# Kernel tuning notes

Measured on AMD Instinct MI355X. Metric: run time of the kernel, lower is better.

The kernel has to match this reference:

```python
import jax, jax.numpy as jnp
import numpy as np

EMBD_DIM = 1024
HEAD_SIZE = 64


def setup_inputs() -> dict:
    key = jax.random.key(0)
    kx, kq, kk, kv = jax.random.split(key, 4)
    x = jax.random.normal(kx, (4, 4096, EMBD_DIM), dtype=jnp.float32)
    # nn.Linear(embd_dim, head_size, bias=False) weights, stored as [C, H] so x @ W
    s = 1.0 / np.sqrt(EMBD_DIM)
    Wq = jax.random.uniform(kq, (EMBD_DIM, HEAD_SIZE), jnp.float32, -s, s)
    Wk = jax.random.uniform(kk, (EMBD_DIM, HEAD_SIZE), jnp.float32, -s, s)
    Wv = jax.random.uniform(kv, (EMBD_DIM, HEAD_SIZE), jnp.float32, -s, s)
    return {"x": x, "Wq": Wq, "Wk": Wk, "Wv": Wv}


def reference(x, Wq, Wk, Wv):
    # q,k,v: [B, T, H]
    q = jnp.einsum("btc,ch->bth", x, Wq)
    k = jnp.einsum("btc,ch->bth", x, Wk)
    v = jnp.einsum("btc,ch->bth", x, Wv)
    scale = k.shape[-1] ** -0.5
    # full [B, T, T] score matrix, as in the original naive implementation
    scores = jnp.einsum("bth,bsh->bts", q, k) * scale
    attn = jax.nn.softmax(scores, axis=-1)
    # dropout p=0.0 -> identity
    out = jnp.einsum("bts,bsh->bth", attn, v)  # [B, T, H]
    return out
```

## Files before the change

kernel.cpp:

```cpp
#include <hip/hip_runtime.h>
#include <hip/hip_bf16.h>

#define B_ 4
#define T_ 4096
#define C_ 1024
#define H_ 64

typedef float  f32x4  __attribute__((ext_vector_type(4)));
typedef short  bf16x8 __attribute__((ext_vector_type(8)));
typedef uint   u32x4  __attribute__((ext_vector_type(4)));

static __device__ __forceinline__ ushort f2bf(float f) {
  union { float f; uint u; } v; v.f = f;
  uint u = v.u;
  u += 0x7FFFu + ((u >> 16) & 1u);
  return (ushort)(u >> 16);
}

static __device__ __forceinline__ uint cvtpk(float s0, float s1) {
  uint r;
  asm("v_cvt_pk_bf16_f32 %0, %1, %2" : "=v"(r) : "v"(s0), "v"(s1));
  return r;
}

static __device__ __forceinline__ void gload_lds16(const void* g, void* l) {
  __builtin_amdgcn_global_load_lds(
      (const __attribute__((address_space(1))) unsigned int*)g,
      (__attribute__((address_space(3))) unsigned int*)l, 16, 0, 0);
}

#define MFMA(a, b, c) __builtin_amdgcn_mfma_f32_16x16x32_bf16(a, b, c, 0, 0, 0)

__global__ __launch_bounds__(256) void wt_prep(const float* __restrict__ Wq,
                                               const float* __restrict__ Wk,
                                               const float* __restrict__ Wv,
                                               ushort* __restrict__ WtF) {
  int idx = blockIdx.x * 256 + threadIdx.x;
  int j = idx & 7, lane = (idx >> 3) & 63, nt = (idx >> 9) & 3;
  int kc = (idx >> 11) & 1, c64 = (idx >> 12) & 15, w = idx >> 16;
  int l15 = lane & 15, g = lane >> 4;
  int c = c64 * 64 + kc * 32 + g * 8 + j;
  int n = nt * 16 + l15;
  const float* W = (w == 0) ? Wq : (w == 1) ? Wk : Wv;
  WtF[idx] = f2bf(W[c * 64 + n]);
}

__global__ __launch_bounds__(256) void qkv_proj(const float* __restrict__ x,
                                                const ushort* __restrict__ WtF,
                                                ushort* __restrict__ Qg,
                                                char* __restrict__ KaF,
                                                char* __restrict__ VaF) {
  __shared__ __align__(16) ushort wl[2][12288];
  const int tid = threadIdx.x;
  const int lane = tid & 63, wid = tid >> 6;
  const int l15 = lane & 15, g = lane >> 4;
  const int b = blockIdx.x >> 6, rt = blockIdx.x & 63;
  const int wrow = rt * 64 + wid * 16;

  f32x4 acc[3][4];
  #pragma unroll
  for (int w = 0; w < 3; w++)
    #pragma unroll
    for (int nt = 0; nt < 4; nt++) acc[w][nt] = (f32x4)0.0f;

  const float* xr = x + ((size_t)b * T_ + wrow + l15) * C_ + g * 8;

  auto stagew = [&](int buf, int c64) {
    char* dst = (char*)wl[buf] + tid * 16;
    const char* src = (const char*)WtF + (size_t)c64 * 8192 + tid * 16;
    #pragma unroll
    for (int p = 0; p < 6; p++)
      gload_lds16(src + (p >> 1) * 131072 + (p & 1) * 4096, dst + p * 4096);
  };

  f32x4 xp[3][4];
  auto xload = [&](int slot, int t) {
    const float* src = xr + t * 64;
    xp[slot][0] = *(const f32x4*)src;
    xp[slot][1] = *(const f32x4*)(src + 4);
    xp[slot][2] = *(const f32x4*)(src + 32);
    xp[slot][3] = *(const f32x4*)(src + 36);
  };

  stagew(0, 0);
  xload(0, 0);
  xload(1, 1);
  asm volatile("s_waitcnt vmcnt(8)" ::: "memory");
  __builtin_amdgcn_s_barrier();
  __builtin_amdgcn_sched_barrier(0);

  #pragma unroll
  for (int t = 0; t < 16; t++) {
    const int cur = t & 1;
    if (t < 15) stagew(cur ^ 1, t + 1);
    if (t < 14) xload((t + 2) % 3, t + 2);

    const int slot = t % 3;
    bf16x8 xa[2];
    #pragma unroll
    for (int kc = 0; kc < 2; kc++) {
      union { uint u[4]; bf16x8 v; } h;
      f32x4 c0 = xp[slot][2 * kc], c1 = xp[slot][2 * kc + 1];
      h.u[0] = cvtpk(c0[0], c0[1]); h.u[1] = cvtpk(c0[2], c0[3]);
      h.u[2] = cvtpk(c1[0], c1[1]); h.u[3] = cvtpk(c1[2], c1[3]);
      xa[kc] = h.v;
    }
    const char* wb = (const char*)wl[cur] + lane * 16;
    __builtin_amdgcn_s_setprio(1);
    #pragma unroll
    for (int w = 0; w < 3; w++)
      #pragma unroll
      for (int kc = 0; kc < 2; kc++)
        #pragma unroll
        for (int nt = 0; nt < 4; nt++) {
          bf16x8 wf = *(const bf16x8*)(wb + w * 8192 + kc * 4096 + nt * 1024);
          acc[w][nt] = MFMA(xa[kc], wf, acc[w][nt]);
        }
    __builtin_amdgcn_s_setprio(0);

    if (t < 15) {
      if (t < 14) asm volatile("s_waitcnt vmcnt(4)" ::: "memory");
      else        asm volatile("s_waitcnt vmcnt(0)" ::: "memory");
      __builtin_amdgcn_s_barrier();
      __builtin_amdgcn_sched_barrier(0);
    }
  }

  char* kdst = KaF + ((size_t)b * 64 + rt) * 8192;
  char* vdst = VaF + ((size_t)b * 128 + (wrow >> 5)) * 4096;
  #pragma unroll
  for (int nt = 0; nt < 4; nt++) {
    int n = nt * 16 + l15;
    int kc = n >> 5, gp2 = (n >> 3) & 3, j2 = n & 7;
    #pragma unroll
    for (int r = 0; r < 4; r++) {
      int tt = wrow + g * 4 + r;
      Qg[((size_t)b * T_ + tt) * H_ + n] = f2bf(acc[0][nt][r]);
      int key = tt & 63;
      *(ushort*)(kdst + kc * 4096 + (key >> 4) * 1024 +
                 (gp2 * 16 + (key & 15)) * 16 + j2 * 2) = f2bf(acc[1][nt][r]);
      int k5 = tt & 31;
      int gp = ((k5 >> 4) << 1) | ((k5 >> 2) & 1);
      int js = ((k5 >> 3) & 1) * 4 + (k5 & 3);
      *(ushort*)(vdst + nt * 1024 + (gp * 16 + l15) * 16 + js * 2) = f2bf(acc[2][nt][r]);
    }
  }
}

__global__ __launch_bounds__(256, 2) void attn(const ushort* __restrict__ Qg,
                                               const char* __restrict__ KaF,
                                               const char* __restrict__ VaF,
                                               float* __restrict__ Op,
                                               float* __restrict__ Ds,
                                               float* __restrict__ out,
                                               int KT) {
  const int tid = threadIdx.x;
  const int lane = tid & 63, wid = tid >> 6;
  const int bid = blockIdx.x;
  const int b = bid & 3;
  const int r2 = bid >> 2;
  const int qt = r2 & 31, s = r2 >> 5;
  const int l15 = lane & 15, g = lane >> 4;

  bf16x8 qa[2][2];
  #pragma unroll
  for (int qs = 0; qs < 2; qs++) {
    const ushort* qp = Qg + ((size_t)b * T_ + qt * 128 + wid * 32 + qs * 16 + l15) * H_ + g * 8;
    qa[qs][0] = *(const bf16x8*)qp;
    qa[qs][1] = *(const bf16x8*)(qp + 32);
  }

  f32x4 oacc[2][4];
  #pragma unroll
  for (int qs = 0; qs < 2; qs++)
    #pragma unroll
    for (int nt = 0; nt < 4; nt++) oacc[qs][nt] = (f32x4)0.0f;
  float dsum[2] = {0.f, 0.f};

  const char* kbase = KaF + (size_t)b * 64 * 8192;
  const char* vbase = VaF + (size_t)b * 128 * 4096;
  const int it0 = s * KT;

  bf16x8 kaA[8], kaB[8];
  {
    const char* kt = kbase + (size_t)it0 * 8192 + lane * 16;
    #pragma unroll
    for (int i = 0; i < 8; i++) kaA[i] = *(const bf16x8*)(kt + i * 1024);
  }

  auto body = [&](int it, bf16x8 (&kaC)[8], bf16x8 (&kaN)[8]) {
    const char* vt = vbase + (size_t)(it0 + it) * 8192 + lane * 16;
    bf16x8 va[8];
    #pragma unroll
    for (int i = 0; i < 8; i++) va[i] = *(const bf16x8*)(vt + i * 1024);

    f32x4 sacc[2][4];
    #pragma unroll
    for (int qs = 0; qs < 2; qs++)
      #pragma unroll
      for (int nt = 0; nt < 4; nt++) sacc[qs][nt] = (f32x4)0.0f;
    __builtin_amdgcn_s_setprio(1);
    #pragma unroll
    for (int nt = 0; nt < 4; nt++)
      #pragma unroll
      for (int qs = 0; qs < 2; qs++) {
        sacc[qs][nt] = MFMA(kaC[nt], qa[qs][0], sacc[qs][nt]);
        sacc[qs][nt] = MFMA(kaC[4 + nt], qa[qs][1], sacc[qs][nt]);
      }
    __builtin_amdgcn_s_setprio(0);

    if (it + 1 < KT) {
      const char* kt = kbase + (size_t)(it0 + it + 1) * 8192 + lane * 16;
      #pragma unroll
      for (int i = 0; i < 8; i++) kaN[i] = *(const bf16x8*)(kt + i * 1024);
    }

    uint t0[2][4], t1[2][4];
    #pragma unroll
    for (int qs = 0; qs < 2; qs++)
      #pragma unroll
      for (int nt = 0; nt < 4; nt++) {
        float p0 = __builtin_amdgcn_exp2f(sacc[qs][nt][0] * 0.18033688011112042f);
        float p1 = __builtin_amdgcn_exp2f(sacc[qs][nt][1] * 0.18033688011112042f);
        float p2 = __builtin_amdgcn_exp2f(sacc[qs][nt][2] * 0.18033688011112042f);
        float p3 = __builtin_amdgcn_exp2f(sacc[qs][nt][3] * 0.18033688011112042f);
        dsum[qs] += (p0 + p1) + (p2 + p3);
        t0[qs][nt] = cvtpk(p0, p1);
        t1[qs][nt] = cvtpk(p2, p3);
      }

    #pragma unroll
    for (int kk = 0; kk < 2; kk++) {
      bf16x8 pf[2];
      #pragma unroll
      for (int qs = 0; qs < 2; qs++) {
        uint x0 = t0[qs][2 * kk], y0 = t0[qs][2 * kk + 1];
        uint x1 = t1[qs][2 * kk], y1 = t1[qs][2 * kk + 1];
        asm volatile("v_permlane32_swap_b32 %0, %1" : "+v"(x0), "+v"(y0));
        asm volatile("v_permlane32_swap_b32 %0, %1" : "+v"(x1), "+v"(y1));
        union { uint u[4]; bf16x8 v; } pfu;
        pfu.u[0] = x0; pfu.u[1] = x1; pfu.u[2] = y0; pfu.u[3] = y1;
        pf[qs] = pfu.v;
      }
      __builtin_amdgcn_s_setprio(1);
      #pragma unroll
      for (int ntd = 0; ntd < 4; ntd++) {
        oacc[0][ntd] = MFMA(va[kk * 4 + ntd], pf[0], oacc[0][ntd]);
        oacc[1][ntd] = MFMA(va[kk * 4 + ntd], pf[1], oacc[1][ntd]);
      }
      __builtin_amdgcn_s_setprio(0);
    }
  };

  for (int it = 0; it < KT; it += 2) {
    body(it, kaA, kaB);
    body(it + 1, kaB, kaA);
  }

  #pragma unroll
  for (int qs = 0; qs < 2; qs++) {
    float d = dsum[qs];
    d += __shfl_xor(d, 16, 64);
    d += __shfl_xor(d, 32, 64);
    const int q = qt * 128 + wid * 32 + qs * 16 + l15;
    if (Op != nullptr) {
      float* ob = Op + ((size_t)(s * 4 + b) * T_ + q) * H_;
      #pragma unroll
      for (int nt = 0; nt < 4; nt++)
        #pragma unroll
        for (int r = 0; r < 4; r++) ob[nt * 16 + g * 4 + r] = oacc[qs][nt][r];
      if (g == 0) Ds[(size_t)(s * 4 + b) * T_ + q] = d;
    } else {
      float inv = 1.0f / d;
      float* ob = out + ((size_t)b * T_ + q) * H_;
      #pragma unroll
      for (int nt = 0; nt < 4; nt++)
        #pragma unroll
        for (int r = 0; r < 4; r++) ob[nt * 16 + g * 4 + r] = oacc[qs][nt][r] * inv;
    }
  }
}

__global__ __launch_bounds__(256) void reduce_seg(const float* __restrict__ Op,
                                                  const float* __restrict__ Ds,
                                                  float* __restrict__ out, int seg) {
  int i = blockIdx.x * 256 + threadIdx.x;
  size_t e = (size_t)i * 4;
  int row = (int)(e >> 6);
  f32x4 o = (f32x4)0.0f;
  float d = 0.0f;
  for (int s = 0; s < seg; s++) {
    o += *(const f32x4*)(Op + (size_t)s * (4u * T_ * H_) + e);
    d += Ds[(size_t)s * (4u * T_) + row];
  }
  *(f32x4*)(out + e) = o * (1.0f / d);
}

extern "C" void kernel_launch(void* const* d_in, const int* in_sizes, int n_in,
                              void* d_out, int out_size, void* d_ws, size_t ws_size,
                              hipStream_t stream) {
  const float* x  = (const float*)d_in[0];
  const float* Wq = (const float*)d_in[1];
  const float* Wk = (const float*)d_in[2];
  const float* Wv = (const float*)d_in[3];
  float* out = (float*)d_out;

  char* ws = (char*)d_ws;
  size_t off = 0;
  auto take = [&](size_t n) -> void* {
    void* p = ws + off;
    off = (off + n + 255) & ~(size_t)255;
    return p;
  };
  ushort* Qg  = (ushort*)take((size_t)B_ * T_ * H_ * 2);
  char*   KaF = (char*)take((size_t)B_ * T_ * H_ * 2);
  char*   VaF = (char*)take((size_t)B_ * T_ * H_ * 2);
  ushort* WtF = (ushort*)take((size_t)3 * H_ * C_ * 2);

  int seg = 1;
  float* Op = nullptr;
  float* Ds = nullptr;
  for (int sg = 4; sg >= 2; sg >>= 1) {
    size_t need = off + (size_t)sg * B_ * T_ * H_ * 4 + 256 + (size_t)sg * B_ * T_ * 4 + 256;
    if (need <= ws_size) {
      seg = sg;
      Op = (float*)take((size_t)sg * B_ * T_ * H_ * 4);
      Ds = (float*)take((size_t)sg * B_ * T_ * 4);
      break;
    }
  }
  int KT = 64 / seg;

  wt_prep<<<768, 256, 0, stream>>>(Wq, Wk, Wv, WtF);
  qkv_proj<<<B_ * 64, 256, 0, stream>>>(x, WtF, Qg, KaF, VaF);
  attn<<<B_ * (T_ / 128) * seg, 256, 0, stream>>>(Qg, KaF, VaF, Op, Ds, out, KT);
  if (Op) reduce_seg<<<(B_ * T_ * H_ / 4 + 255) / 256, 256, 0, stream>>>(Op, Ds, out, seg);
}
```

Baseline: 54.88 us.

## Stage K/V tiles in double-buffered LDS and double per-block query tile

The attention kernel now has each block cover 256 queries, with each wave handling 64, instead of 128. K and V tiles are copied from global memory into a double-buffered LDS area with direct global-to-LDS loads, and waves read their MFMA operands from LDS, so one tile fetch is shared by four waves. The split over key segments rises to 8 when the workspace allows, which keeps the grid large enough. In exchange it adds a barrier and a full vmcnt wait on every iteration, more accumulator registers per wave (which may lower occupancy with launch bounds of 2), and more partial results for the reduction kernel to combine.

```diff
diff --git a/kernel.cpp b/kernel.cpp
--- a/kernel.cpp
+++ b/kernel.cpp
@@ -154,70 +154,74 @@
                                                float* __restrict__ Ds,
                                                float* __restrict__ out,
                                                int KT) {
+  __shared__ __align__(16) char kv[2][16384];
   const int tid = threadIdx.x;
   const int lane = tid & 63, wid = tid >> 6;
   const int bid = blockIdx.x;
   const int b = bid & 3;
-  const int r2 = bid >> 2;
-  const int qt = r2 & 31, s = r2 >> 5;
+  const int qt = (bid >> 2) & 15, s = bid >> 6;
   const int l15 = lane & 15, g = lane >> 4;
 
-  bf16x8 qa[2][2];
-  #pragma unroll
-  for (int qs = 0; qs < 2; qs++) {
-    const ushort* qp = Qg + ((size_t)b * T_ + qt * 128 + wid * 32 + qs * 16 + l15) * H_ + g * 8;
+  bf16x8 qa[4][2];
+  #pragma unroll
+  for (int qs = 0; qs < 4; qs++) {
+    const ushort* qp = Qg + ((size_t)b * T_ + qt * 256 + wid * 64 + qs * 16 + l15) * H_ + g * 8;
     qa[qs][0] = *(const bf16x8*)qp;
     qa[qs][1] = *(const bf16x8*)(qp + 32);
   }
 
-  f32x4 oacc[2][4];
-  #pragma unroll
-  for (int qs = 0; qs < 2; qs++)
+  f32x4 oacc[4][4];
+  #pragma unroll
+  for (int qs = 0; qs < 4; qs++)
     #pragma unroll
     for (int nt = 0; nt < 4; nt++) oacc[qs][nt] = (f32x4)0.0f;
-  float dsum[2] = {0.f, 0.f};
+  float dsum[4] = {0.f, 0.f, 0.f, 0.f};
 
   const char* kbase = KaF + (size_t)b * 64 * 8192;
   const char* vbase = VaF + (size_t)b * 128 * 4096;
   const int it0 = s * KT;
 
-  bf16x8 kaA[8], kaB[8];
-  {
-    const char* kt = kbase + (size_t)it0 * 8192 + lane * 16;
-    #pragma unroll
-    for (int i = 0; i < 8; i++) kaA[i] = *(const bf16x8*)(kt + i * 1024);
-  }
-
-  auto body = [&](int it, bf16x8 (&kaC)[8], bf16x8 (&kaN)[8]) {
-    const char* vt = vbase + (size_t)(it0 + it) * 8192 + lane * 16;
-    bf16x8 va[8];
-    #pragma unroll
-    for (int i = 0; i < 8; i++) va[i] = *(const bf16x8*)(vt + i * 1024);
-
-    f32x4 sacc[2][4];
-    #pragma unroll
-    for (int qs = 0; qs < 2; qs++)
+  auto stage = [&](int buf, int it) {
+    char* dst = kv[buf] + tid * 16;
+    const char* ks = kbase + (size_t)it * 8192 + tid * 16;
+    const char* vs = vbase + (size_t)it * 8192 + tid * 16;
+    gload_lds16(ks, dst);
+    gload_lds16(ks + 4096, dst + 4096);
+    gload_lds16(vs, dst + 8192);
+    gload_lds16(vs + 4096, dst + 12288);
+  };
+
+  stage(0, it0);
+  asm volatile("s_waitcnt vmcnt(0)" ::: "memory");
+  __builtin_amdgcn_s_barrier();
+  __builtin_amdgcn_sched_barrier(0);
+
+  for (int it = 0; it < KT; it++) {
+    const int cur = it & 1;
+    if (it + 1 < KT) stage(cur ^ 1, it0 + it + 1);
+    const char* kl = kv[cur];
+    const char* vl = kv[cur] + 8192;
+
+    f32x4 sacc[4][4];
+    #pragma unroll
+    for (int qs = 0; qs < 4; qs++)
       #pragma unroll
       for (int nt = 0; nt < 4; nt++) sacc[qs][nt] = (f32x4)0.0f;
     __builtin_amdgcn_s_setprio(1);
     #pragma unroll
     for (int nt = 0; nt < 4; nt++)
       #pragma unroll
-      for (int qs = 0; qs < 2; qs++) {
-        sacc[qs][nt] = MFMA(kaC[nt], qa[qs][0], sacc[qs][nt]);
-        sacc[qs][nt] = MFMA(kaC[4 + nt], qa[qs][1], sacc[qs][nt]);
+      for (int kc = 0; kc < 2; kc++) {
+        bf16x8 ka = *(const bf16x8*)(kl + kc * 4096 + nt * 1024 + lane * 16);
+        #pragma unroll
+        for (int qs = 0; qs < 4; qs++)
+          sacc[qs][nt] = MFMA(ka, qa[qs][kc], sacc[qs][nt]);
       }
     __builtin_amdgcn_s_setprio(0);
 
-    if (it + 1 < KT) {
-      const char* kt = kbase + (size_t)(it0 + it + 1) * 8192 + lane * 16;
-      #pragma unroll
-      for (int i = 0; i < 8; i++) kaN[i] = *(const bf16x8*)(kt + i * 1024);
-    }
-
-    uint t0[2][4], t1[2][4];
-    #pragma unroll
-    for (int qs = 0; qs < 2; qs++)
+    uint t0[4][4], t1[4][4];
+    #pragma unroll
+    for (int qs = 0; qs < 4; qs++)
       #pragma unroll
       for (int nt = 0; nt < 4; nt++) {
         float p0 = __builtin_amdgcn_exp2f(sacc[qs][nt][0] * 0.18033688011112042f);
@@ -231,9 +235,9 @@
 
     #pragma unroll
     for (int kk = 0; kk < 2; kk++) {
-      bf16x8 pf[2];
-      #pragma unroll
-      for (int qs = 0; qs < 2; qs++) {
+      bf16x8 pf[4];
+      #pragma unroll
+      for (int qs = 0; qs < 4; qs++) {
         uint x0 = t0[qs][2 * kk], y0 = t0[qs][2 * kk + 1];
         uint x1 = t1[qs][2 * kk], y1 = t1[qs][2 * kk + 1];
         asm volatile("v_permlane32_swap_b32 %0, %1" : "+v"(x0), "+v"(y0));
@@ -245,24 +249,27 @@
       __builtin_amdgcn_s_setprio(1);
       #pragma unroll
       for (int ntd = 0; ntd < 4; ntd++) {
-        oacc[0][ntd] = MFMA(va[kk * 4 + ntd], pf[0], oacc[0][ntd]);
-        oacc[1][ntd] = MFMA(va[kk * 4 + ntd], pf[1], oacc[1][ntd]);
+        bf16x8 va = *(const bf16x8*)(vl + kk * 4096 + ntd * 1024 + lane * 16);
+        #pragma unroll
+        for (int qs = 0; qs < 4; qs++)
+          oacc[qs][ntd] = MFMA(va, pf[qs], oacc[qs][ntd]);
       }
       __builtin_amdgcn_s_setprio(0);
     }
-  };
-
-  for (int it = 0; it < KT; it += 2) {
-    body(it, kaA, kaB);
-    body(it + 1, kaB, kaA);
-  }
-
-  #pragma unroll
-  for (int qs = 0; qs < 2; qs++) {
+
+    if (it + 1 < KT) {
+      asm volatile("s_waitcnt vmcnt(0)" ::: "memory");
+      __builtin_amdgcn_s_barrier();
+      __builtin_amdgcn_sched_barrier(0);
+    }
+  }
+
+  #pragma unroll
+  for (int qs = 0; qs < 4; qs++) {
     float d = dsum[qs];
     d += __shfl_xor(d, 16, 64);
     d += __shfl_xor(d, 32, 64);
-    const int q = qt * 128 + wid * 32 + qs * 16 + l15;
+    const int q = qt * 256 + wid * 64 + qs * 16 + l15;
     if (Op != nullptr) {
       float* ob = Op + ((size_t)(s * 4 + b) * T_ + q) * H_;
       #pragma unroll
@@ -320,7 +327,7 @@
   int seg = 1;
   float* Op = nullptr;
   float* Ds = nullptr;
-  for (int sg = 4; sg >= 2; sg >>= 1) {
+  for (int sg = 8; sg >= 2; sg >>= 1) {
     size_t need = off + (size_t)sg * B_ * T_ * H_ * 4 + 256 + (size_t)sg * B_ * T_ * 4 + 256;
     if (need <= ws_size) {
       seg = sg;
@@ -333,6 +340,6 @@
 
   wt_prep<<<768, 256, 0, stream>>>(Wq, Wk, Wv, WtF);
   qkv_proj<<<B_ * 64, 256, 0, stream>>>(x, WtF, Qg, KaF, VaF);
-  attn<<<B_ * (T_ / 128) * seg, 256, 0, stream>>>(Qg, KaF, VaF, Op, Ds, out, KT);
+  attn<<<B_ * (T_ / 256) * seg, 256, 0, stream>>>(Qg, KaF, VaF, Op, Ds, out, KT);
   if (Op) reduce_seg<<<(B_ * T_ * H_ / 4 + 255) / 256, 256, 0, stream>>>(Op, Ds, out, seg);
 }
```

Result: slower. 60.21 us (+9.7%).

## Stage K/V tiles through LDS with triple-buffered async loads; bf16 partials

Applied to the files above, without the earlier changes.

The attention kernel now copies each K/V tile into a three-slot LDS ring using global_load_lds, staged two iterations ahead, with waitcnt and barriers between iterations. Previously each wave loaded K and V straight into registers. The LDS path shares one tile load across the four waves and cuts VGPR pressure. The split-K partial outputs are now written as bf16 instead of fp32, which halves the traffic to and from reduce_seg but loses some precision. wt_prep is also reorganised so its reads of the weights are coalesced, with the layout transform moved to the write side. The per-iteration barriers add synchronisation cost.

```diff
diff --git a/kernel.cpp b/kernel.cpp
--- a/kernel.cpp
+++ b/kernel.cpp
@@ -36,13 +36,14 @@
                                                const float* __restrict__ Wv,
                                                ushort* __restrict__ WtF) {
   int idx = blockIdx.x * 256 + threadIdx.x;
-  int j = idx & 7, lane = (idx >> 3) & 63, nt = (idx >> 9) & 3;
-  int kc = (idx >> 11) & 1, c64 = (idx >> 12) & 15, w = idx >> 16;
-  int l15 = lane & 15, g = lane >> 4;
-  int c = c64 * 64 + kc * 32 + g * 8 + j;
-  int n = nt * 16 + l15;
+  int w = idx >> 16, idx2 = idx & 65535;
+  int c = idx2 >> 6, n = idx2 & 63;
   const float* W = (w == 0) ? Wq : (w == 1) ? Wk : Wv;
-  WtF[idx] = f2bf(W[c * 64 + n]);
+  float v = W[idx2];
+  int c64 = c >> 6, kc = (c >> 5) & 1, g = (c >> 3) & 3, j = c & 7;
+  int nt = n >> 4, l15 = n & 15;
+  size_t dst = ((size_t)((((w * 16 + c64) * 2 + kc) * 4 + nt) * 64 + g * 16 + l15)) * 8 + j;
+  WtF[dst] = f2bf(v);
 }
 
 __global__ __launch_bounds__(256) void qkv_proj(const float* __restrict__ x,
@@ -150,16 +151,16 @@
 __global__ __launch_bounds__(256, 2) void attn(const ushort* __restrict__ Qg,
                                                const char* __restrict__ KaF,
                                                const char* __restrict__ VaF,
-                                               float* __restrict__ Op,
+                                               ushort* __restrict__ Op,
                                                float* __restrict__ Ds,
                                                float* __restrict__ out,
                                                int KT) {
+  __shared__ __align__(16) char kv[3][16384];
   const int tid = threadIdx.x;
   const int lane = tid & 63, wid = tid >> 6;
   const int bid = blockIdx.x;
   const int b = bid & 3;
-  const int r2 = bid >> 2;
-  const int qt = r2 & 31, s = r2 >> 5;
+  const int qt = (bid >> 2) & 31, s = bid >> 7;
   const int l15 = lane & 15, g = lane >> 4;
 
   bf16x8 qa[2][2];
@@ -181,18 +182,28 @@
   const char* vbase = VaF + (size_t)b * 128 * 4096;
   const int it0 = s * KT;
 
-  bf16x8 kaA[8], kaB[8];
-  {
-    const char* kt = kbase + (size_t)it0 * 8192 + lane * 16;
-    #pragma unroll
-    for (int i = 0; i < 8; i++) kaA[i] = *(const bf16x8*)(kt + i * 1024);
-  }
-
-  auto body = [&](int it, bf16x8 (&kaC)[8], bf16x8 (&kaN)[8]) {
-    const char* vt = vbase + (size_t)(it0 + it) * 8192 + lane * 16;
-    bf16x8 va[8];
-    #pragma unroll
-    for (int i = 0; i < 8; i++) va[i] = *(const bf16x8*)(vt + i * 1024);
+  auto stage = [&](int buf, int it) {
+    char* dst = kv[buf] + tid * 16;
+    const char* ks = kbase + (size_t)it * 8192 + tid * 16;
+    const char* vs = vbase + (size_t)it * 8192 + tid * 16;
+    gload_lds16(ks, dst);
+    gload_lds16(ks + 4096, dst + 4096);
+    gload_lds16(vs, dst + 8192);
+    gload_lds16(vs + 4096, dst + 12288);
+  };
+
+  stage(0, it0);
+  stage(1, it0 + 1);
+  asm volatile("s_waitcnt vmcnt(4)" ::: "memory");
+  __builtin_amdgcn_s_barrier();
+  __builtin_amdgcn_sched_barrier(0);
+
+  int cur = 0;
+  for (int it = 0; it < KT; it++) {
+    int pf = cur + 2; if (pf >= 3) pf -= 3;
+    if (it + 2 < KT) stage(pf, it0 + it + 2);
+    const char* kl = kv[cur];
+    const char* vl = kv[cur] + 8192;
 
     f32x4 sacc[2][4];
     #pragma unroll
@@ -203,17 +214,12 @@
     #pragma unroll
     for (int nt = 0; nt < 4; nt++)
       #pragma unroll
-      for (int qs = 0; qs < 2; qs++) {
-        sacc[qs][nt] = MFMA(kaC[nt], qa[qs][0], sacc[qs][nt]);
-        sacc[qs][nt] = MFMA(kaC[4 + nt], qa[qs][1], sacc[qs][nt]);
+      for (int kc = 0; kc < 2; kc++) {
+        bf16x8 ka = *(const bf16x8*)(kl + kc * 4096 + nt * 1024 + lane * 16);
+        sacc[0][nt] = MFMA(ka, qa[0][kc], sacc[0][nt]);
+        sacc[1][nt] = MFMA(ka, qa[1][kc], sacc[1][nt]);
       }
     __builtin_amdgcn_s_setprio(0);
-
-    if (it + 1 < KT) {
-      const char* kt = kbase + (size_t)(it0 + it + 1) * 8192 + lane * 16;
-      #pragma unroll
-      for (int i = 0; i < 8; i++) kaN[i] = *(const bf16x8*)(kt + i * 1024);
-    }
 
     uint t0[2][4], t1[2][4];
     #pragma unroll
@@ -231,7 +237,7 @@
 
     #pragma unroll
     for (int kk = 0; kk < 2; kk++) {
-      bf16x8 pf[2];
+      bf16x8 pf2[2];
       #pragma unroll
       for (int qs = 0; qs < 2; qs++) {
         uint x0 = t0[qs][2 * kk], y0 = t0[qs][2 * kk + 1];
@@ -240,21 +246,25 @@
         asm volatile("v_permlane32_swap_b32 %0, %1" : "+v"(x1), "+v"(y1));
         union { uint u[4]; bf16x8 v; } pfu;
         pfu.u[0] = x0; pfu.u[1] = x1; pfu.u[2] = y0; pfu.u[3] = y1;
-        pf[qs] = pfu.v;
+        pf2[qs] = pfu.v;
       }
       __builtin_amdgcn_s_setprio(1);
       #pragma unroll
       for (int ntd = 0; ntd < 4; ntd++) {
-        oacc[0][ntd] = MFMA(va[kk * 4 + ntd], pf[0], oacc[0][ntd]);
-        oacc[1][ntd] = MFMA(va[kk * 4 + ntd], pf[1], oacc[1][ntd]);
+        bf16x8 va = *(const bf16x8*)(vl + kk * 4096 + ntd * 1024 + lane * 16);
+        oacc[0][ntd] = MFMA(va, pf2[0], oacc[0][ntd]);
+        oacc[1][ntd] = MFMA(va, pf2[1], oacc[1][ntd]);
       }
       __builtin_amdgcn_s_setprio(0);
     }
-  };
-
-  for (int it = 0; it < KT; it += 2) {
-    body(it, kaA, kaB);
-    body(it + 1, kaB, kaA);
+
+    if (it + 1 < KT) {
+      if (it + 2 < KT) asm volatile("s_waitcnt vmcnt(4)" ::: "memory");
+      else             asm volatile("s_waitcnt vmcnt(0)" ::: "memory");
+      __builtin_amdgcn_s_barrier();
+      __builtin_amdgcn_sched_barrier(0);
+    }
+    cur = cur + 1; if (cur >= 3) cur -= 3;
   }
 
   #pragma unroll
@@ -264,11 +274,14 @@
     d += __shfl_xor(d, 32, 64);
     const int q = qt * 128 + wid * 32 + qs * 16 + l15;
     if (Op != nullptr) {
-      float* ob = Op + ((size_t)(s * 4 + b) * T_ + q) * H_;
-      #pragma unroll
-      for (int nt = 0; nt < 4; nt++)
-        #pragma unroll
-        for (int r = 0; r < 4; r++) ob[nt * 16 + g * 4 + r] = oacc[qs][nt][r];
+      ushort* ob = Op + ((size_t)(s * 4 + b) * T_ + q) * H_;
+      #pragma unroll
+      for (int nt = 0; nt < 4; nt++) {
+        uint2 pk;
+        pk.x = cvtpk(oacc[qs][nt][0], oacc[qs][nt][1]);
+        pk.y = cvtpk(oacc[qs][nt][2], oacc[qs][nt][3]);
+        *(uint2*)(ob + nt * 16 + g * 4) = pk;
+      }
       if (g == 0) Ds[(size_t)(s * 4 + b) * T_ + q] = d;
     } else {
       float inv = 1.0f / d;
@@ -281,7 +294,7 @@
   }
 }
 
-__global__ __launch_bounds__(256) void reduce_seg(const float* __restrict__ Op,
+__global__ __launch_bounds__(256) void reduce_seg(const ushort* __restrict__ Op,
                                                   const float* __restrict__ Ds,
                                                   float* __restrict__ out, int seg) {
   int i = blockIdx.x * 256 + threadIdx.x;
@@ -290,8 +303,12 @@
   f32x4 o = (f32x4)0.0f;
   float d = 0.0f;
   for (int s = 0; s < seg; s++) {
-    o += *(const f32x4*)(Op + (size_t)s * (4u * T_ * H_) + e);
-    d += Ds[(size_t)s * (4u * T_) + row];
+    uint2 pk = *(const uint2*)(Op + (size_t)s * ((size_t)B_ * T_ * H_) + e);
+    union { uint u; float f; } c0, c1, c2, c3;
+    c0.u = (pk.x & 0xFFFFu) << 16; c1.u = (pk.x >> 16) << 16;
+    c2.u = (pk.y & 0xFFFFu) << 16; c3.u = (pk.y >> 16) << 16;
+    o[0] += c0.f; o[1] += c1.f; o[2] += c2.f; o[3] += c3.f;
+    d += Ds[(size_t)s * ((size_t)B_ * T_) + row];
   }
   *(f32x4*)(out + e) = o * (1.0f / d);
 }
@@ -318,13 +335,13 @@
   ushort* WtF = (ushort*)take((size_t)3 * H_ * C_ * 2);
 
   int seg = 1;
-  float* Op = nullptr;
+  ushort* Op = nullptr;
   float* Ds = nullptr;
   for (int sg = 4; sg >= 2; sg >>= 1) {
-    size_t need = off + (size_t)sg * B_ * T_ * H_ * 4 + 256 + (size_t)sg * B_ * T_ * 4 + 256;
+    size_t need = off + (size_t)sg * B_ * T_ * H_ * 2 + 256 + (size_t)sg * B_ * T_ * 4 + 256;
     if (need <= ws_size) {
       seg = sg;
-      Op = (float*)take((size_t)sg * B_ * T_ * H_ * 4);
+      Op = (ushort*)take((size_t)sg * B_ * T_ * H_ * 2);
       Ds = (float*)take((size_t)sg * B_ * T_ * 4);
       break;
     }
```

Result: no change. 55.60 us (+1.3%).
